# Optimization experiments

Measured on AMD Instinct MI355X. Metric: run time of the kernel, lower is better.

Reference implementation:

```python
import jax, jax.numpy as jnp
import numpy as np

HIDDEN = 2048
N_HEADS = 32
N_KV_HEADS = 8
HEAD_DIM = HIDDEN // N_HEADS  # 64
GROUP = N_HEADS // N_KV_HEADS  # 4
BATCH = 2
SEQ = 2048


def setup_inputs() -> dict:
    key = jax.random.key(0)
    ks = jax.random.split(key, 9)
    s_in = 1.0 / np.sqrt(HIDDEN)
    X = jax.random.normal(ks[0], (BATCH, SEQ, HIDDEN), dtype=jnp.float32)
    Wq = jax.random.uniform(ks[1], (HIDDEN, N_HEADS * HEAD_DIM), jnp.float32, -s_in, s_in)
    bq = jax.random.uniform(ks[2], (N_HEADS * HEAD_DIM,), jnp.float32, -s_in, s_in)
    Wk = jax.random.uniform(ks[3], (HIDDEN, N_KV_HEADS * HEAD_DIM), jnp.float32, -s_in, s_in)
    bk = jax.random.uniform(ks[4], (N_KV_HEADS * HEAD_DIM,), jnp.float32, -s_in, s_in)
    Wv = jax.random.uniform(ks[5], (HIDDEN, N_KV_HEADS * HEAD_DIM), jnp.float32, -s_in, s_in)
    bv = jax.random.uniform(ks[6], (N_KV_HEADS * HEAD_DIM,), jnp.float32, -s_in, s_in)
    Wo = jax.random.uniform(ks[7], (HIDDEN, HIDDEN), jnp.float32, -s_in, s_in)
    bo = jax.random.uniform(ks[8], (HIDDEN,), jnp.float32, -s_in, s_in)
    return {"X": X, "Wq": Wq, "bq": bq, "Wk": Wk, "bk": bk,
            "Wv": Wv, "bv": bv, "Wo": Wo, "bo": bo}


def reference(X, Wq, bq, Wk, bk, Wv, bv, Wo, bo):
    B, S, _ = X.shape
    q = (X @ Wq + bq).reshape(B, S, N_HEADS, HEAD_DIM).transpose(0, 2, 1, 3)      # [B,H,S,D]
    k = (X @ Wk + bk).reshape(B, S, N_KV_HEADS, HEAD_DIM).transpose(0, 2, 1, 3)   # [B,Hkv,S,D]
    v = (X @ Wv + bv).reshape(B, S, N_KV_HEADS, HEAD_DIM).transpose(0, 2, 1, 3)
    # repeat_interleave KV heads to match query heads (GQA expansion)
    k = jnp.repeat(k, GROUP, axis=1)  # [B,H,S,D]
    v = jnp.repeat(v, GROUP, axis=1)
    scale = 1.0 / np.sqrt(HEAD_DIM).astype(np.float32)
    scores = jnp.einsum("bhqd,bhkd->bhqk", q, k) * scale  # [B,H,S,S]
    weights = jax.nn.softmax(scores, axis=-1)
    out = jnp.einsum("bhqk,bhkd->bhqd", weights, v)        # [B,H,S,D]
    out = out.transpose(0, 2, 1, 3).reshape(B, S, HIDDEN)
    return out @ Wo + bo
```

## Files before the change

### kernel.cpp

```cpp
#include <hip/hip_runtime.h>
#include <hip/hip_bf16.h>

#define HID 2048
#define NH 32
#define NKV 8
#define HD 64
#define BB 2
#define SS_ 2048
#define MM (BB * SS_)

#define QT 256
#define KT 64
#define LDK 72
#define LDV 68
#define LDO 66

typedef unsigned short u16;
typedef __attribute__((ext_vector_type(8)))  short bf16x8;
typedef __attribute__((ext_vector_type(4)))  float f32x4;
typedef __attribute__((ext_vector_type(16))) float f32x16;
typedef __attribute__((ext_vector_type(2)))  unsigned int u32x2;

__device__ __forceinline__ u16 f2bf(float f) {
    union { float f; unsigned int i; } v; v.f = f;
    unsigned int lsb = (v.i >> 16) & 1u;
    v.i += 0x7fffu + lsb;
    return (u16)(v.i >> 16);
}
__device__ __forceinline__ unsigned int pack_bf2(float lo, float hi) {
    return ((unsigned int)f2bf(hi) << 16) | (unsigned int)f2bf(lo);
}
__device__ __forceinline__ unsigned int pack_rtz(float lo, float hi) {
    return __builtin_amdgcn_perm(__float_as_uint(hi), __float_as_uint(lo), 0x07060302u);
}
__device__ __forceinline__ void gload16(const u16* g, u16* l) {
    __builtin_amdgcn_global_load_lds(
        (const __attribute__((address_space(1))) void*)(u16*)g,
        (__attribute__((address_space(3))) void*)l, 16, 0, 0);
}

__global__ __launch_bounds__(256) void cvt_kernel(
    const float* __restrict__ in, u16* __restrict__ out, int n4)
{
    const int i = blockIdx.x * 256 + threadIdx.x;
    if (i < n4) {
        float4 f = ((const float4*)in)[i];
        ushort4 r;
        r.x = f2bf(f.x); r.y = f2bf(f.y); r.z = f2bf(f.z); r.w = f2bf(f.w);
        ((ushort4*)out)[i] = r;
    }
}

__global__ __launch_bounds__(256) void tw_kernel(
    const float* __restrict__ Wq, const float* __restrict__ Wk,
    const float* __restrict__ Wv, const float* __restrict__ Wo,
    u16* __restrict__ Tq, u16* __restrict__ Tk,
    u16* __restrict__ Tv, u16* __restrict__ To)
{
    __shared__ float tile[64][65];
    const int by = blockIdx.y;
    const float* W; u16* T; int N, n0;
    if (by < 32)      { W = Wq; T = Tq; N = 2048; n0 = by * 64; }
    else if (by < 40) { W = Wk; T = Tk; N = 512;  n0 = (by - 32) * 64; }
    else if (by < 48) { W = Wv; T = Tv; N = 512;  n0 = (by - 40) * 64; }
    else              { W = Wo; T = To; N = 2048; n0 = (by - 48) * 64; }
    const int k0 = blockIdx.x * 64;
    const int r  = threadIdx.x >> 2;
    const int c0 = (threadIdx.x & 3) << 4;
    #pragma unroll
    for (int u = 0; u < 4; ++u) {
        float4 f = *(const float4*)&W[(size_t)(k0 + r) * N + n0 + c0 + u * 4];
        tile[r][c0 + u * 4 + 0] = f.x; tile[r][c0 + u * 4 + 1] = f.y;
        tile[r][c0 + u * 4 + 2] = f.z; tile[r][c0 + u * 4 + 3] = f.w;
    }
    __syncthreads();
    #pragma unroll
    for (int u = 0; u < 4; ++u) {
        ushort4 o;
        o.x = f2bf(tile[c0 + u * 4 + 0][r]);
        o.y = f2bf(tile[c0 + u * 4 + 1][r]);
        o.z = f2bf(tile[c0 + u * 4 + 2][r]);
        o.w = f2bf(tile[c0 + u * 4 + 3][r]);
        *(ushort4*)&T[(size_t)(n0 + r) * HID + k0 + c0 + u * 4] = o;
    }
}

__global__ __launch_bounds__(256) void proj_kernel(
    const u16* __restrict__ Xb,
    const u16* __restrict__ Tq, const u16* __restrict__ Tk, const u16* __restrict__ Tv,
    const float* __restrict__ bq, const float* __restrict__ bk, const float* __restrict__ bv,
    u16* __restrict__ qo, u16* __restrict__ ko, u16* __restrict__ vo)
{
    __shared__ __align__(16) u16 Al[128][32];
    __shared__ __align__(16) u16 Bl[128][32];
    const int tid = threadIdx.x;
    const int w = tid >> 6, l15 = tid & 15, lg = (tid & 63) >> 4;
    const int wr = w >> 1, wc = w & 1;
    const int m0 = blockIdx.x * 128;
    const int n0 = blockIdx.y * 128;

    const u16* Bt; const float* bias; u16* dst; int nh, nb;
    if (n0 < 2048)      { Bt = Tq + (size_t)n0 * HID;          bias = bq + n0;          dst = qo; nh = NH;  nb = n0; }
    else if (n0 < 2560) { Bt = Tk + (size_t)(n0 - 2048) * HID; bias = bk + (n0 - 2048); dst = ko; nh = NKV; nb = n0 - 2048; }
    else                { Bt = Tv + (size_t)(n0 - 2560) * HID; bias = bv + (n0 - 2560); dst = vo; nh = NKV; nb = n0 - 2560; }

    const int L    = tid & 63;
    const int lrow = L >> 2;
    const int sdat = (L & 3) ^ (lrow & 3);
    const int arow = w * 32 + lrow;
    const int sw   = (lg ^ (l15 & 3)) * 8;

    f32x4 acc[4][4] = {};
    for (int k0 = 0; k0 < HID; k0 += 32) {
        gload16(&Xb[(size_t)(m0 + arow) * HID + k0 + sdat * 8],      &Al[w * 32][0]);
        gload16(&Xb[(size_t)(m0 + arow + 16) * HID + k0 + sdat * 8], &Al[w * 32 + 16][0]);
        gload16(&Bt[(size_t)(arow) * HID + k0 + sdat * 8],           &Bl[w * 32][0]);
        gload16(&Bt[(size_t)(arow + 16) * HID + k0 + sdat * 8],      &Bl[w * 32 + 16][0]);
        __syncthreads();
        bf16x8 af[4], bfr[4];
        #pragma unroll
        for (int i = 0; i < 4; ++i) {
            af[i]  = *(const bf16x8*)&Al[wr * 64 + i * 16 + l15][sw];
            bfr[i] = *(const bf16x8*)&Bl[wc * 64 + i * 16 + l15][sw];
        }
        #pragma unroll
        for (int mf = 0; mf < 4; ++mf)
            #pragma unroll
            for (int nf = 0; nf < 4; ++nf)
                acc[mf][nf] = __builtin_amdgcn_mfma_f32_16x16x32_bf16(af[mf], bfr[nf], acc[mf][nf], 0, 0, 0);
        __syncthreads();
    }

    #pragma unroll
    for (int nf = 0; nf < 4; ++nf) {
        const int cl = nb + wc * 64 + nf * 16 + l15;
        const int hh = cl >> 6, dd = cl & 63;
        const float bv_ = bias[wc * 64 + nf * 16 + l15];
        #pragma unroll
        for (int mf = 0; mf < 4; ++mf)
            #pragma unroll
            for (int r = 0; r < 4; ++r) {
                const int m = m0 + wr * 64 + mf * 16 + lg * 4 + r;
                const int bb_ = m >> 11, ss = m & (SS_ - 1);
                dst[(((size_t)bb_ * nh + hh) * SS_ + ss) * HD + dd] = f2bf(acc[mf][nf][r] + bv_);
            }
    }
}

__global__ __launch_bounds__(512, 4) void attn_kernel(
    const u16* __restrict__ q, const u16* __restrict__ k,
    const u16* __restrict__ v, u16* __restrict__ o)
{
    union SMem {
        struct { u16 Ks[2][KT][LDK]; u16 Vt[2][HD][LDV]; } s;
        u16 Ot[QT][LDO];
    };
    __shared__ SMem sm;

    const int tid = threadIdx.x;
    const int w   = tid >> 6;
    const int l   = tid & 63;
    const int l31 = l & 31;
    const int hi  = l >> 5;
    const int qt  = blockIdx.x;
    const int h   = blockIdx.y;
    const int b   = blockIdx.z;
    const int hk  = h >> 2;

    const u16* qb = q + (((size_t)b * NH  + h ) * SS_ + qt * QT) * HD;
    const u16* kp = k + (((size_t)b * NKV + hk) * SS_) * HD;
    const u16* vp = v + (((size_t)b * NKV + hk) * SS_) * HD;

    bf16x8 qf[4];
    #pragma unroll
    for (int kc = 0; kc < 4; ++kc)
        qf[kc] = *(const bf16x8*)&qb[(size_t)(w * 32 + l31) * HD + kc * 16 + hi * 8];

    f32x16 oaccT[2] = {};
    float d0s = 0.f, d1s = 0.f, d2s = 0.f, d3s = 0.f;
    const float C = 0.1803368801f;

    const int krow = tid >> 3, kcol = (tid & 7) << 3;
    const int vk0  = (tid & 31) << 1, vd0 = (tid >> 5) << 2;

    const int NT = SS_ / KT;

    {
        bf16x8 kr0 = *(const bf16x8*)&kp[(size_t)krow * HD + kcol];
        uint2 vv[2];
        #pragma unroll
        for (int i = 0; i < 2; ++i)
            vv[i] = *(const uint2*)&vp[(size_t)(vk0 + i) * HD + vd0];
        *(bf16x8*)&sm.s.Ks[0][krow][kcol] = kr0;
        #pragma unroll
        for (int j = 0; j < 4; ++j) {
            ushort2 tv;
            tv.x = ((const u16*)&vv[0])[j];
            tv.y = ((const u16*)&vv[1])[j];
            *(ushort2*)&sm.s.Vt[0][vd0 + j][vk0] = tv;
        }
    }
    __syncthreads();

    int p = 0;
    for (int t = 0; t < NT; ++t) {
        const int tn = (t + 1 < NT) ? (t + 1) : (NT - 1);
        bf16x8 nk0 = *(const bf16x8*)&kp[(size_t)(tn * KT + krow) * HD + kcol];
        uint2 nv[2];
        #pragma unroll
        for (int i = 0; i < 2; ++i)
            nv[i] = *(const uint2*)&vp[(size_t)(tn * KT + vk0 + i) * HD + vd0];

        f32x16 st[2] = {};
        __builtin_amdgcn_s_setprio(1);
        #pragma unroll
        for (int kb = 0; kb < 2; ++kb)
            #pragma unroll
            for (int kc = 0; kc < 4; ++kc) {
                bf16x8 kf = *(const bf16x8*)&sm.s.Ks[p][kb * 32 + l31][kc * 16 + hi * 8];
                st[kb] = __builtin_amdgcn_mfma_f32_32x32x16_bf16(kf, qf[kc], st[kb], 0, 0, 0);
            }
        __builtin_amdgcn_s_setprio(0);

        #pragma unroll
        for (int kb = 0; kb < 2; ++kb)
            #pragma unroll
            for (int r = 0; r < 16; r += 4) {
                const float p0 = exp2f(st[kb][r + 0] * C);
                const float p1 = exp2f(st[kb][r + 1] * C);
                const float p2 = exp2f(st[kb][r + 2] * C);
                const float p3 = exp2f(st[kb][r + 3] * C);
                st[kb][r + 0] = p0; st[kb][r + 1] = p1;
                st[kb][r + 2] = p2; st[kb][r + 3] = p3;
                d0s += p0; d1s += p1; d2s += p2; d3s += p3;
            }

        #pragma unroll
        for (int kc = 0; kc < 4; ++kc) {
            const int kb = kc >> 1, c4 = (kc & 1) * 4;
            const unsigned int a0 = pack_rtz(st[kb][2 * (c4 + 0)], st[kb][2 * (c4 + 0) + 1]);
            const unsigned int a1 = pack_rtz(st[kb][2 * (c4 + 1)], st[kb][2 * (c4 + 1) + 1]);
            const unsigned int a2 = pack_rtz(st[kb][2 * (c4 + 2)], st[kb][2 * (c4 + 2) + 1]);
            const unsigned int a3 = pack_rtz(st[kb][2 * (c4 + 3)], st[kb][2 * (c4 + 3) + 1]);
            u32x2 r0 = __builtin_amdgcn_permlane32_swap(a0, a2, false, false);
            u32x2 r1 = __builtin_amdgcn_permlane32_swap(a1, a3, false, false);
            uint4 pbu;
            pbu.x = r0.x;
            pbu.y = r1.x;
            pbu.z = r0.y;
            pbu.w = r1.y;
            bf16x8 pb = *(bf16x8*)&pbu;
            __builtin_amdgcn_s_setprio(1);
            #pragma unroll
            for (int db = 0; db < 2; ++db) {
                bf16x8 vf = *(const bf16x8*)&sm.s.Vt[p][db * 32 + l31][kc * 16 + hi * 8];
                oaccT[db] = __builtin_amdgcn_mfma_f32_32x32x16_bf16(vf, pb, oaccT[db], 0, 0, 0);
            }
            __builtin_amdgcn_s_setprio(0);
        }

        if (t + 1 < NT) {
            *(bf16x8*)&sm.s.Ks[p ^ 1][krow][kcol] = nk0;
            #pragma unroll
            for (int j = 0; j < 4; ++j) {
                ushort2 tv;
                tv.x = ((const u16*)&nv[0])[j];
                tv.y = ((const u16*)&nv[1])[j];
                *(ushort2*)&sm.s.Vt[p ^ 1][vd0 + j][vk0] = tv;
            }
        }
        __syncthreads();
        p ^= 1;
    }

    float l_i = (d0s + d1s) + (d2s + d3s);
    l_i += __shfl_xor(l_i, 32);
    const float inv = 1.0f / l_i;

    #pragma unroll
    for (int db = 0; db < 2; ++db)
        #pragma unroll
        for (int pp = 0; pp < 8; ++pp) {
            const int d0 = db * 32 + 2 * (pp & 1) + 4 * hi + 8 * (pp >> 1);
            unsigned int r_ = pack_bf2(oaccT[db][2 * pp] * inv, oaccT[db][2 * pp + 1] * inv);
            *(unsigned int*)&sm.Ot[w * 32 + l31][d0] = r_;
        }
    __syncthreads();
    {
        const int row = tid >> 1, half = tid & 1;
        u16* go = o + ((size_t)b * SS_ + qt * QT + row) * HID + h * HD + half * 32;
        #pragma unroll
        for (int u = 0; u < 2; ++u) {
            uint4 t0 = *(uint4*)&sm.Ot[row][half * 32 + u * 16];
            *(uint4*)&go[u * 16] = t0;
            uint4 t1 = *(uint4*)&sm.Ot[row][half * 32 + u * 16 + 8];
            *(uint4*)&go[u * 16 + 8] = t1;
        }
    }
}

__global__ __launch_bounds__(256) void oproj_kernel(
    const u16* __restrict__ Ab, const u16* __restrict__ To,
    const float* __restrict__ bo, float* __restrict__ out)
{
    __shared__ __align__(16) u16 Al[128][32];
    __shared__ __align__(16) u16 Bl[128][32];
    const int tid = threadIdx.x;
    const int w = tid >> 6, l15 = tid & 15, lg = (tid & 63) >> 4;
    const int wr = w >> 1, wc = w & 1;
    const int m0 = blockIdx.x * 128;
    const int n0 = blockIdx.y * 128;
    const u16* Bt = To + (size_t)n0 * HID;

    const int L    = tid & 63;
    const int lrow = L >> 2;
    const int sdat = (L & 3) ^ (lrow & 3);
    const int arow = w * 32 + lrow;
    const int sw   = (lg ^ (l15 & 3)) * 8;

    f32x4 acc[4][4] = {};
    for (int k0 = 0; k0 < HID; k0 += 32) {
        gload16(&Ab[(size_t)(m0 + arow) * HID + k0 + sdat * 8],      &Al[w * 32][0]);
        gload16(&Ab[(size_t)(m0 + arow + 16) * HID + k0 + sdat * 8], &Al[w * 32 + 16][0]);
        gload16(&Bt[(size_t)(arow) * HID + k0 + sdat * 8],           &Bl[w * 32][0]);
        gload16(&Bt[(size_t)(arow + 16) * HID + k0 + sdat * 8],      &Bl[w * 32 + 16][0]);
        __syncthreads();
        bf16x8 af[4], bfr[4];
        #pragma unroll
        for (int i = 0; i < 4; ++i) {
            af[i]  = *(const bf16x8*)&Al[wr * 64 + i * 16 + l15][sw];
            bfr[i] = *(const bf16x8*)&Bl[wc * 64 + i * 16 + l15][sw];
        }
        #pragma unroll
        for (int mf = 0; mf < 4; ++mf)
            #pragma unroll
            for (int nf = 0; nf < 4; ++nf)
                acc[mf][nf] = __builtin_amdgcn_mfma_f32_16x16x32_bf16(af[mf], bfr[nf], acc[mf][nf], 0, 0, 0);
        __syncthreads();
    }

    #pragma unroll
    for (int nf = 0; nf < 4; ++nf) {
        const int col = n0 + wc * 64 + nf * 16 + l15;
        const float bv_ = bo[col];
        #pragma unroll
        for (int mf = 0; mf < 4; ++mf)
            #pragma unroll
            for (int r = 0; r < 4; ++r) {
                const int m = m0 + wr * 64 + mf * 16 + lg * 4 + r;
                out[(size_t)m * HID + col] = acc[mf][nf][r] + bv_;
            }
    }
}

extern "C" void kernel_launch(void* const* d_in, const int* in_sizes, int n_in,
                              void* d_out, int out_size, void* d_ws, size_t ws_size,
                              hipStream_t stream) {
    int iX = 0, iWq = 1, ibq = 2, iWk = 3, ibk = 4, iWv = 5, ibv = 6, iWo = 7, ibo = 8;
    if (n_in == 9 && in_sizes[1] == 1048576) {
        iWk = 1; iWo = 2; iWq = 3; iWv = 4; ibk = 5; ibo = 6; ibq = 7; ibv = 8;
    }
    const float* X  = (const float*)d_in[iX];
    const float* Wq = (const float*)d_in[iWq];
    const float* bq = (const float*)d_in[ibq];
    const float* Wk = (const float*)d_in[iWk];
    const float* bk = (const float*)d_in[ibk];
    const float* Wv = (const float*)d_in[iWv];
    const float* bv = (const float*)d_in[ibv];
    const float* Wo = (const float*)d_in[iWo];
    const float* bo = (const float*)d_in[ibo];
    float* out = (float*)d_out;

    u16* Xb  = (u16*)d_ws;
    u16* Tq  = Xb  + (size_t)MM * HID;
    u16* Tk  = Tq  + (size_t)HID * HID;
    u16* Tv  = Tk  + (size_t)512 * HID;
    u16* To  = Tv  + (size_t)512 * HID;
    u16* qws = To  + (size_t)HID * HID;
    u16* kws = qws + (size_t)BB * NH  * SS_ * HD;
    u16* vws = kws + (size_t)BB * NKV * SS_ * HD;
    u16* ows = vws + (size_t)BB * NKV * SS_ * HD;

    cvt_kernel<<<dim3((MM * HID / 4 + 255) / 256), 256, 0, stream>>>(X, Xb, MM * HID / 4);
    tw_kernel<<<dim3(32, 80), 256, 0, stream>>>(Wq, Wk, Wv, Wo, Tq, Tk, Tv, To);
    proj_kernel<<<dim3(32, 24), 256, 0, stream>>>(Xb, Tq, Tk, Tv, bq, bk, bv, qws, kws, vws);
    attn_kernel<<<dim3(SS_ / QT, 32, 2), 512, 0, stream>>>(qws, kws, vws, ows);
    oproj_kernel<<<dim3(32, 16), 256, 0, stream>>>(ows, To, bo, out);
}
```

Before: 305.7 us.

## Split KV sequence across two attention blocks and combine partial outputs

Splits each attention tile's key/value range into two halves handled by separate blocks, doubling grid size from 512 to 1024 blocks. Each split writes a normalized partial output and its row sum. A new combine kernel merges the two partials, weighting each by its share of the total row sum. This aims to improve GPU fill and occupancy, at the cost of an extra kernel, extra partial-output traffic and one more bf16 rounding. The Xb and Tq buffers are reused as scratch space.

Result: slower. 324.1 us (+6.0%).

```diff
diff --git a/kernel.cpp b/kernel.cpp
--- a/kernel.cpp
+++ b/kernel.cpp
@@ -11,6 +11,8 @@
 
 #define QT 256
 #define KT 64
+#define NSPLIT 2
+#define KVS (SS_ / NSPLIT)
 #define LDK 72
 #define LDV 68
 #define LDO 66
@@ -26,6 +28,9 @@
     unsigned int lsb = (v.i >> 16) & 1u;
     v.i += 0x7fffu + lsb;
     return (u16)(v.i >> 16);
+}
+__device__ __forceinline__ float bf2f(u16 u) {
+    union { unsigned int i; float f; } v; v.i = ((unsigned int)u) << 16; return v.f;
 }
 __device__ __forceinline__ unsigned int pack_bf2(float lo, float hi) {
     return ((unsigned int)f2bf(hi) << 16) | (unsigned int)f2bf(lo);
@@ -149,7 +154,8 @@
 
 __global__ __launch_bounds__(512, 4) void attn_kernel(
     const u16* __restrict__ q, const u16* __restrict__ k,
-    const u16* __restrict__ v, u16* __restrict__ o)
+    const u16* __restrict__ v, u16* __restrict__ o0,
+    u16* __restrict__ o1, float* __restrict__ ls)
 {
     union SMem {
         struct { u16 Ks[2][KT][LDK]; u16 Vt[2][HD][LDV]; } s;
@@ -164,12 +170,15 @@
     const int hi  = l >> 5;
     const int qt  = blockIdx.x;
     const int h   = blockIdx.y;
-    const int b   = blockIdx.z;
+    const int bz  = blockIdx.z;
+    const int b   = bz >> 1;
+    const int s   = bz & 1;
     const int hk  = h >> 2;
 
     const u16* qb = q + (((size_t)b * NH  + h ) * SS_ + qt * QT) * HD;
-    const u16* kp = k + (((size_t)b * NKV + hk) * SS_) * HD;
-    const u16* vp = v + (((size_t)b * NKV + hk) * SS_) * HD;
+    const u16* kp = k + (((size_t)b * NKV + hk) * SS_ + s * KVS) * HD;
+    const u16* vp = v + (((size_t)b * NKV + hk) * SS_ + s * KVS) * HD;
+    u16* dst = s ? o1 : o0;
 
     bf16x8 qf[4];
     #pragma unroll
@@ -183,7 +192,7 @@
     const int krow = tid >> 3, kcol = (tid & 7) << 3;
     const int vk0  = (tid & 31) << 1, vd0 = (tid >> 5) << 2;
 
-    const int NT = SS_ / KT;
+    const int NT = KVS / KT;
 
     {
         bf16x8 kr0 = *(const bf16x8*)&kp[(size_t)krow * HD + kcol];
@@ -277,6 +286,9 @@
     l_i += __shfl_xor(l_i, 32);
     const float inv = 1.0f / l_i;
 
+    if (hi == 0)
+        ls[(((size_t)s * BB + b) * NH + h) * SS_ + qt * QT + w * 32 + l31] = l_i;
+
     #pragma unroll
     for (int db = 0; db < 2; ++db)
         #pragma unroll
@@ -288,7 +300,7 @@
     __syncthreads();
     {
         const int row = tid >> 1, half = tid & 1;
-        u16* go = o + ((size_t)b * SS_ + qt * QT + row) * HID + h * HD + half * 32;
+        u16* go = dst + ((size_t)b * SS_ + qt * QT + row) * HID + h * HD + half * 32;
         #pragma unroll
         for (int u = 0; u < 2; ++u) {
             uint4 t0 = *(uint4*)&sm.Ot[row][half * 32 + u * 16];
@@ -297,6 +309,36 @@
             *(uint4*)&go[u * 16 + 8] = t1;
         }
     }
+}
+
+__global__ __launch_bounds__(256) void comb_kernel(
+    u16* __restrict__ o0, const u16* __restrict__ o1, const float* __restrict__ ls)
+{
+    const size_t idx = ((size_t)blockIdx.x * 256 + threadIdx.x) * 8;
+    const int row  = (int)(idx >> 11);
+    const int col  = (int)(idx & 2047);
+    const int b    = row >> 11;
+    const int qrow = row & (SS_ - 1);
+    const int h    = col >> 6;
+    const float l0 = ls[(((size_t)0 * BB + b) * NH + h) * SS_ + qrow];
+    const float l1 = ls[(((size_t)1 * BB + b) * NH + h) * SS_ + qrow];
+    const float inv = 1.0f / (l0 + l1);
+    const float r0 = l0 * inv, r1 = l1 * inv;
+    ushort4 x0 = *(const ushort4*)&o0[idx];
+    ushort4 x1 = *(const ushort4*)&o0[idx + 4];
+    ushort4 y0 = *(const ushort4*)&o1[idx];
+    ushort4 y1 = *(const ushort4*)&o1[idx + 4];
+    ushort4 z0, z1;
+    z0.x = f2bf(r0 * bf2f(x0.x) + r1 * bf2f(y0.x));
+    z0.y = f2bf(r0 * bf2f(x0.y) + r1 * bf2f(y0.y));
+    z0.z = f2bf(r0 * bf2f(x0.z) + r1 * bf2f(y0.z));
+    z0.w = f2bf(r0 * bf2f(x0.w) + r1 * bf2f(y0.w));
+    z1.x = f2bf(r0 * bf2f(x1.x) + r1 * bf2f(y1.x));
+    z1.y = f2bf(r0 * bf2f(x1.y) + r1 * bf2f(y1.y));
+    z1.z = f2bf(r0 * bf2f(x1.z) + r1 * bf2f(y1.z));
+    z1.w = f2bf(r0 * bf2f(x1.w) + r1 * bf2f(y1.w));
+    *(ushort4*)&o0[idx]     = z0;
+    *(ushort4*)&o0[idx + 4] = z1;
 }
 
 __global__ __launch_bounds__(256) void oproj_kernel(
@@ -380,10 +422,13 @@
     u16* kws = qws + (size_t)BB * NH  * SS_ * HD;
     u16* vws = kws + (size_t)BB * NKV * SS_ * HD;
     u16* ows = vws + (size_t)BB * NKV * SS_ * HD;
+    u16*   po1 = Xb;
+    float* ls  = (float*)Tq;
 
     cvt_kernel<<<dim3((MM * HID / 4 + 255) / 256), 256, 0, stream>>>(X, Xb, MM * HID / 4);
     tw_kernel<<<dim3(32, 80), 256, 0, stream>>>(Wq, Wk, Wv, Wo, Tq, Tk, Tv, To);
     proj_kernel<<<dim3(32, 24), 256, 0, stream>>>(Xb, Tq, Tk, Tv, bq, bk, bv, qws, kws, vws);
-    attn_kernel<<<dim3(SS_ / QT, 32, 2), 512, 0, stream>>>(qws, kws, vws, ows);
+    attn_kernel<<<dim3(SS_ / QT, 32, BB * NSPLIT), 512, 0, stream>>>(qws, kws, vws, ows, po1, ls);
+    comb_kernel<<<dim3((int)((size_t)MM * HID / 8 / 256)), 256, 0, stream>>>(ows, po1, ls);
     oproj_kernel<<<dim3(32, 16), 256, 0, stream>>>(ows, To, bo, out);
 }
```
